# Performance work log

Measured on AMD Instinct MI355X. Metric: run time of the kernel, lower is better.

Reference implementation:

```python
import jax, jax.numpy as jnp
import numpy as np

B = 256      # number of graphs (args.batch_size)
NPG = 1000   # nodes per graph (args.num_node)
C = 64       # in_channels
DEG = 16     # avg degree
K = 500      # ceil(ratio * NPG), ratio = 0.5
EPS = 1e-8


def setup_inputs() -> dict:
    key = jax.random.key(0)
    k1, k2, k3, k4, k5 = jax.random.split(key, 5)
    N = B * NPG
    epg = NPG * DEG  # edges per graph
    x = jax.random.normal(k1, (N, C), jnp.float32)
    src = jax.random.randint(k2, (B, epg), 0, NPG)
    dst = jax.random.randint(k3, (B, epg), 0, NPG)
    off = (jnp.arange(B, dtype=jnp.int32) * NPG)[:, None]
    edge_index = jnp.stack([(src + off).reshape(-1), (dst + off).reshape(-1)]).astype(jnp.int32)
    edge_attr = jax.random.uniform(k4, (B * epg,), jnp.float32)
    batch = jnp.repeat(jnp.arange(B, dtype=jnp.int32), NPG)
    W = jax.random.normal(k5, (C, C), jnp.float32) * (1.0 / np.sqrt(C))
    b = jnp.zeros((C,), jnp.float32)
    return {"istraining": 1, "x": x, "edge_index": edge_index, "edge_attr": edge_attr,
            "batch": batch, "W": W, "b": b}


def _gcn_conv(x, edge_index, W, b):
    # PyG GCNConv: x' = D^{-1/2} (A + I) D^{-1/2} X W + b, unit edge weights.
    N = x.shape[0]
    sl = jnp.arange(N, dtype=edge_index.dtype)
    src = jnp.concatenate([edge_index[0], sl])  # message source j
    dst = jnp.concatenate([edge_index[1], sl])  # aggregation target i
    deg = jnp.zeros((N,), x.dtype).at[dst].add(1.0)
    dinv = jnp.where(deg > 0, jax.lax.rsqrt(jnp.maximum(deg, 1.0)), 0.0)
    norm = dinv[src] * dinv[dst]          # [E+N]
    h = x @ W                              # [N, C]
    msg = h[src] * norm[:, None]           # gather + scale (dominant traffic)
    out = jax.ops.segment_sum(msg, dst, num_segments=N) + b
    return out


def _node_score(x):
    # compute_node_score: cosine similarity of each node to its graph centroid
    # (community prototype), plus KL(softmax(score) || uniform) per graph.
    xb = x.reshape(B, NPG, C)
    cen = xb.mean(axis=1, keepdims=True)                       # [B,1,C]
    num = jnp.sum(xb * cen, axis=-1)                           # [B,NPG]
    den = jnp.linalg.norm(xb, axis=-1) * jnp.linalg.norm(cen, axis=-1) + EPS
    score = num / den                                          # [B,NPG]
    logp = jax.nn.log_softmax(score, axis=1)
    kl = jnp.sum(jnp.exp(logp) * (logp + jnp.log(jnp.float32(NPG))), axis=1)  # [B]
    indices_ = jnp.argsort(-score, axis=1)                     # [B,NPG]
    return score, kl, indices_


def reference(istraining, x, edge_index, edge_attr, batch, W, b):
    N = x.shape[0]
    x = _gcn_conv(x, edge_index, W, b)
    score, kl_all_batch, indices_ = _node_score(x)
    # per-graph top-k (fixed k since every graph has NPG nodes)
    _, idx = jax.lax.top_k(score, K)                           # [B,K]
    perm = ((jnp.arange(B, dtype=idx.dtype) * NPG)[:, None] + idx).reshape(-1)  # [B*K]
    score_flat = score.reshape(-1)
    x_new = x[perm] * jnp.tanh(score_flat[perm])[:, None]
    batch_new = batch[perm]
    # filter_adj: keep edges with both endpoints retained, re-index to new ids.
    mapping = jnp.full((N,), -1, dtype=jnp.int32).at[perm].set(
        jnp.arange(perm.shape[0], dtype=jnp.int32))
    new_ei = mapping[edge_index]                               # [2,E], -1 = dropped
    edge_mask = jnp.logical_and(new_ei[0] >= 0, new_ei[1] >= 0)
    edge_attr_new = jnp.where(edge_mask, edge_attr, 0.0)
    return (x_new, new_ei, edge_attr_new, edge_mask, batch_new, perm, kl_all_batch, indices_)
```

## Files before the change

kernel.cpp:

```cpp
#include <hip/hip_runtime.h>
#include <math.h>

#define NPG 1000
#define KTOP 500
#define C 64
#define EPG 16000
#define BPG 63

__device__ __forceinline__ int readlane_i(int v, int l) {
    return (int)__builtin_amdgcn_readlane((unsigned)v, (unsigned)l);
}

__global__ __launch_bounds__(1024) void build_graph_k(const int* __restrict__ ei, int E,
                                                      int* __restrict__ deg,
                                                      float* __restrict__ dinv,
                                                      int* __restrict__ off,
                                                      int* __restrict__ csr,
                                                      float* __restrict__ cen_sum) {
    int g = blockIdx.x, t = threadIdx.x;
    __shared__ int cnt[NPG];
    __shared__ int soff[NPG];
    __shared__ unsigned short lcsr[EPG];
    __shared__ int red[1024];
    const int gbase = g * NPG;
    const int ebase = g * EPG;
    const int* __restrict__ srcp = ei + ebase;
    const int* __restrict__ dstp = ei + E + ebase;

    if (t < C) cen_sum[(size_t)g * C + t] = 0.f;
    for (int i = t; i < NPG; i += 1024) cnt[i] = 0;
    __syncthreads();
    for (int i = t; i < EPG; i += 1024) atomicAdd(&cnt[dstp[i] - gbase], 1);
    __syncthreads();
    int v = (t < NPG) ? cnt[t] : 0;
    red[t] = v;
    __syncthreads();
    for (int o = 1; o < 1024; o <<= 1) {
        int xx = (t >= o) ? red[t - o] : 0;
        __syncthreads();
        red[t] += xx;
        __syncthreads();
    }
    if (t < NPG) soff[t] = red[t] - v;
    __syncthreads();
    for (int i = t; i < NPG; i += 1024) {
        int d = cnt[i];
        deg[gbase + i] = d;
        dinv[gbase + i] = 1.0f / sqrtf((float)(d + 1));
        off[gbase + i] = ebase + soff[i];
    }
    __syncthreads();
    for (int i = t; i < NPG; i += 1024) cnt[i] = soff[i];
    __syncthreads();
    for (int i = t; i < EPG; i += 1024) {
        int d = dstp[i] - gbase;
        int pos = atomicAdd(&cnt[d], 1);
        lcsr[pos] = (unsigned short)(srcp[i] - gbase);
    }
    __syncthreads();
    int4* co = (int4*)(csr + ebase);
    for (int i = t; i < EPG / 4; i += 1024) {
        int4 vv;
        vv.x = gbase + (int)lcsr[i * 4 + 0];
        vv.y = gbase + (int)lcsr[i * 4 + 1];
        vv.z = gbase + (int)lcsr[i * 4 + 2];
        vv.w = gbase + (int)lcsr[i * 4 + 3];
        co[i] = vv;
    }
}

__global__ __launch_bounds__(256) void gemm_k(const float* __restrict__ x,
                                              const float* __restrict__ W,
                                              const float* __restrict__ dinv,
                                              float* __restrict__ h2, int N) {
    __shared__ float sW[C * C];
    int t = threadIdx.x;
    for (int i = t; i < C * C / 4; i += 256) ((float4*)sW)[i] = ((const float4*)W)[i];
    __syncthreads();
    int r0 = blockIdx.x * 512 + t;
    int r1 = r0 + 256;
    if (r0 >= N) return;
    bool has1 = (r1 < N);
    const float4* x0 = (const float4*)(x + (size_t)r0 * C);
    const float4* x1 = (const float4*)(x + (size_t)(has1 ? r1 : r0) * C);
    float acc0[C], acc1[C];
#pragma unroll
    for (int i = 0; i < C; ++i) { acc0[i] = 0.f; acc1[i] = 0.f; }
    float4 a0 = x0[0], a1 = x1[0];
    for (int k4 = 0; k4 < 16; ++k4) {
        float4 b0, b1;
        if (k4 < 15) { b0 = x0[k4 + 1]; b1 = x1[k4 + 1]; }
        const float4* wr = (const float4*)(sW + k4 * 4 * C);
        const float* a0f = (const float*)&a0;
        const float* a1f = (const float*)&a1;
#pragma unroll
        for (int c4 = 0; c4 < 16; ++c4) {
            float4 w[4];
            w[0] = wr[c4]; w[1] = wr[16 + c4]; w[2] = wr[32 + c4]; w[3] = wr[48 + c4];
            const float* wf = (const float*)w;
#pragma unroll
            for (int j = 0; j < 4; ++j) {
                float s0 = acc0[c4 * 4 + j], s1 = acc1[c4 * 4 + j];
#pragma unroll
                for (int kk = 0; kk < 4; ++kk) {
                    float wv = wf[kk * 4 + j];
                    s0 = fmaf(a0f[kk], wv, s0);
                    s1 = fmaf(a1f[kk], wv, s1);
                }
                acc0[c4 * 4 + j] = s0; acc1[c4 * 4 + j] = s1;
            }
        }
        a0 = b0; a1 = b1;
    }
    float dv0 = dinv[r0];
    float dv1 = has1 ? dinv[r1] : 0.f;
#pragma unroll
    for (int i = 0; i < C; ++i) { acc0[i] *= dv0; acc1[i] *= dv1; }
    float4* h0 = (float4*)(h2 + (size_t)r0 * C);
#pragma unroll
    for (int q = 0; q < 16; ++q) h0[q] = ((float4*)acc0)[q];
    if (has1) {
        float4* h1 = (float4*)(h2 + (size_t)r1 * C);
#pragma unroll
        for (int q = 0; q < 16; ++q) h1[q] = ((float4*)acc1)[q];
    }
}

__global__ __launch_bounds__(256) void gather_k(const int* __restrict__ csr,
                                                const int* __restrict__ off,
                                                const int* __restrict__ deg,
                                                const float* __restrict__ h2,
                                                const float* __restrict__ dinv,
                                                const float* __restrict__ bias,
                                                float* __restrict__ out2,
                                                float* __restrict__ cen_sum,
                                                int N, int B) {
    __shared__ float cenacc[C];
    int blk = blockIdx.x;
    int wave = threadIdx.x >> 6;
    int lane = threadIdx.x & 63;
    int t = threadIdx.x;
    int g, blkin;
    if ((B & 7) == 0) {
        int xcd = blk & 7, slot = blk >> 3;
        g = (slot / BPG) * 8 + xcd;
        blkin = slot % BPG;
    } else {
        g = blk / BPG;
        blkin = blk % BPG;
    }
    if (t < C) cenacc[t] = 0.f;
    __syncthreads();

    int base = blkin * 4 + wave;
    if (base < NPG / 4) {
        int nA = g * NPG + base;
        int nB = nA + 250, nC_ = nA + 500, nD = nA + 750;
        int oA = off[nA], oB = off[nB], oC = off[nC_], oD = off[nD];
        int dA = deg[nA], dB = deg[nB], dC = deg[nC_], dD = deg[nD];
        float diA = dinv[nA], diB = dinv[nB], diC = dinv[nC_], diD = dinv[nD];
        float hA = h2[(size_t)nA * C + lane];
        float hB = h2[(size_t)nB * C + lane];
        float hC = h2[(size_t)nC_ * C + lane];
        float hD = h2[(size_t)nD * C + lane];
        float bv = bias[lane];
        int svA = (lane < dA) ? csr[oA + lane] : nA;
        int svB = (lane < dB) ? csr[oB + lane] : nB;
        int svC = (lane < dC) ? csr[oC + lane] : nC_;
        int svD = (lane < dD) ? csr[oD + lane] : nD;
        int jmA = dA < 64 ? dA : 64;
        int jmB = dB < 64 ? dB : 64;
        int jmC = dC < 64 ? dC : 64;
        int jmD = dD < 64 ? dD : 64;
        int rA = (jmA + 3) & ~3, rB = (jmB + 3) & ~3;
        int rC = (jmC + 3) & ~3, rD = (jmD + 3) & ~3;
        int m0 = rA > rB ? rA : rB;
        int m1 = rC > rD ? rC : rD;
        int mmax = m0 > m1 ? m0 : m1;
        float aA = 0.f, aB = 0.f, aC = 0.f, aD = 0.f;
        for (int j = 0; j < mmax; j += 4) {
            if (j < rA) {
                int s0 = readlane_i(svA, j + 0), s1 = readlane_i(svA, j + 1);
                int s2 = readlane_i(svA, j + 2), s3 = readlane_i(svA, j + 3);
                float v0 = h2[(size_t)s0 * C + lane];
                float v1 = h2[(size_t)s1 * C + lane];
                float v2 = h2[(size_t)s2 * C + lane];
                float v3 = h2[(size_t)s3 * C + lane];
                aA += (v0 + v1) + (v2 + v3);
            }
            if (j < rB) {
                int s0 = readlane_i(svB, j + 0), s1 = readlane_i(svB, j + 1);
                int s2 = readlane_i(svB, j + 2), s3 = readlane_i(svB, j + 3);
                float v0 = h2[(size_t)s0 * C + lane];
                float v1 = h2[(size_t)s1 * C + lane];
                float v2 = h2[(size_t)s2 * C + lane];
                float v3 = h2[(size_t)s3 * C + lane];
                aB += (v0 + v1) + (v2 + v3);
            }
            if (j < rC) {
                int s0 = readlane_i(svC, j + 0), s1 = readlane_i(svC, j + 1);
                int s2 = readlane_i(svC, j + 2), s3 = readlane_i(svC, j + 3);
                float v0 = h2[(size_t)s0 * C + lane];
                float v1 = h2[(size_t)s1 * C + lane];
                float v2 = h2[(size_t)s2 * C + lane];
                float v3 = h2[(size_t)s3 * C + lane];
                aC += (v0 + v1) + (v2 + v3);
            }
            if (j < rD) {
                int s0 = readlane_i(svD, j + 0), s1 = readlane_i(svD, j + 1);
                int s2 = readlane_i(svD, j + 2), s3 = readlane_i(svD, j + 3);
                float v0 = h2[(size_t)s0 * C + lane];
                float v1 = h2[(size_t)s1 * C + lane];
                float v2 = h2[(size_t)s2 * C + lane];
                float v3 = h2[(size_t)s3 * C + lane];
                aD += (v0 + v1) + (v2 + v3);
            }
        }
        for (int j = 64; j < dA; ++j) aA += h2[(size_t)csr[oA + j] * C + lane];
        for (int j = 64; j < dB; ++j) aB += h2[(size_t)csr[oB + j] * C + lane];
        for (int j = 64; j < dC; ++j) aC += h2[(size_t)csr[oC + j] * C + lane];
        for (int j = 64; j < dD; ++j) aD += h2[(size_t)csr[oD + j] * C + lane];
        float cA = 1.0f - (float)(rA - jmA);
        float cB = 1.0f - (float)(rB - jmB);
        float cC = 1.0f - (float)(rC - jmC);
        float cD = 1.0f - (float)(rD - jmD);
        float resA = fmaf(diA, fmaf(cA, hA, aA), bv);
        float resB = fmaf(diB, fmaf(cB, hB, aB), bv);
        float resC = fmaf(diC, fmaf(cC, hC, aC), bv);
        float resD = fmaf(diD, fmaf(cD, hD, aD), bv);
        out2[(size_t)nA * C + lane] = resA;
        out2[(size_t)nB * C + lane] = resB;
        out2[(size_t)nC_ * C + lane] = resC;
        out2[(size_t)nD * C + lane] = resD;
        float csum = (resA + resB) + (resC + resD);
        atomicAdd(&cenacc[lane], csum);
    }
    __syncthreads();
    if (t < C) atomicAdd(&cen_sum[(size_t)g * C + t], cenacc[t]);
}

__global__ void cen_fin_k(const float* __restrict__ cen_sum, float* __restrict__ cen,
                          float* __restrict__ cnorm) {
    int g = blockIdx.x, c = threadIdx.x;
    float m = cen_sum[(size_t)g * C + c] * (1.0f / 1000.0f);
    cen[g * C + c] = m;
    float v = m * m;
    for (int o = 32; o > 0; o >>= 1) v += __shfl_down(v, o, 64);
    if (c == 0) cnorm[g] = sqrtf(v);
}

__global__ __launch_bounds__(256) void score2_k(const float* __restrict__ out2,
                                                const float* __restrict__ cen,
                                                const float* __restrict__ cnorm,
                                                float* __restrict__ score, int N) {
    int wave = threadIdx.x >> 6, lane = threadIdx.x & 63;
    int r0 = blockIdx.x * 16 + wave * 4;
    if (r0 >= N) return;
    int g0 = (r0 + 0) / NPG, g1 = (r0 + 1) / NPG;
    int g2 = (r0 + 2) / NPG, g3 = (r0 + 3) / NPG;
    float m0 = cen[g0 * C + lane];
    float m1 = cen[g1 * C + lane];
    float m2 = cen[g2 * C + lane];
    float m3 = cen[g3 * C + lane];
    float a0 = out2[(size_t)(r0 + 0) * C + lane];
    float a1 = out2[(size_t)(r0 + 1) * C + lane];
    float a2 = out2[(size_t)(r0 + 2) * C + lane];
    float a3 = out2[(size_t)(r0 + 3) * C + lane];
    float n0 = a0 * m0, n1 = a1 * m1, n2 = a2 * m2, n3 = a3 * m3;
    float q0 = a0 * a0, q1 = a1 * a1, q2 = a2 * a2, q3 = a3 * a3;
    for (int o = 32; o > 0; o >>= 1) {
        n0 += __shfl_down(n0, o, 64); q0 += __shfl_down(q0, o, 64);
        n1 += __shfl_down(n1, o, 64); q1 += __shfl_down(q1, o, 64);
        n2 += __shfl_down(n2, o, 64); q2 += __shfl_down(q2, o, 64);
        n3 += __shfl_down(n3, o, 64); q3 += __shfl_down(q3, o, 64);
    }
    if (lane == 0) {
        score[r0 + 0] = n0 / (sqrtf(q0) * cnorm[g0] + 1e-8f);
        score[r0 + 1] = n1 / (sqrtf(q1) * cnorm[g1] + 1e-8f);
        score[r0 + 2] = n2 / (sqrtf(q2) * cnorm[g2] + 1e-8f);
        score[r0 + 3] = n3 / (sqrtf(q3) * cnorm[g3] + 1e-8f);
    }
}

__global__ void softmax_kl_k(const float* __restrict__ score, float* __restrict__ o_kl) {
    int g = blockIdx.x, t = threadIdx.x;
    __shared__ float ss[NPG];
    __shared__ float red[256];
    const float4* s4 = (const float4*)(score + (size_t)g * NPG);
    for (int i = t; i < NPG / 4; i += 256) ((float4*)ss)[i] = s4[i];
    __syncthreads();
    float mx = -INFINITY;
    for (int i = t; i < NPG; i += 256) mx = fmaxf(mx, ss[i]);
    red[t] = mx;
    __syncthreads();
    for (int w = 128; w > 0; w >>= 1) { if (t < w) red[t] = fmaxf(red[t], red[t + w]); __syncthreads(); }
    mx = red[0];
    __syncthreads();
    float se = 0.f;
    for (int i = t; i < NPG; i += 256) se += expf(ss[i] - mx);
    red[t] = se;
    __syncthreads();
    for (int w = 128; w > 0; w >>= 1) { if (t < w) red[t] += red[t + w]; __syncthreads(); }
    float lse = logf(red[0]);
    __syncthreads();
    float kl = 0.f;
    const float ln_npg = 6.9077552790f;
    for (int i = t; i < NPG; i += 256) {
        float lp = ss[i] - mx - lse;
        kl += expf(lp) * (lp + ln_npg);
    }
    red[t] = kl;
    __syncthreads();
    for (int w = 128; w > 0; w >>= 1) { if (t < w) red[t] += red[t + w]; __syncthreads(); }
    if (t == 0) o_kl[g] = red[0];
}

__global__ __launch_bounds__(1024) void sort_k(const float* __restrict__ score,
                                               int* __restrict__ sidx,
                                               int* __restrict__ mapping,
                                               float* __restrict__ o_perm,
                                               float* __restrict__ o_batch,
                                               float* __restrict__ o_ind) {
    __shared__ unsigned long long kk[1024];
    int g = blockIdx.x, t = threadIdx.x;
    const int gbase = g * NPG;
    unsigned long long v;
    if (t < NPG) {
        unsigned u = __float_as_uint(score[(size_t)gbase + t]);
        u = (u & 0x80000000u) ? ~u : (u | 0x80000000u);
        v = ((unsigned long long)(~u) << 32) | (unsigned)t;
    } else {
        v = ~0ULL;
    }
    kk[t] = v;
    __syncthreads();
    for (int k = 2; k <= 1024; k <<= 1) {
        for (int j = k >> 1; j > 0; j >>= 1) {
            int ixj = t ^ j;
            if (ixj > t) {
                unsigned long long a = kk[t], b = kk[ixj];
                bool up = ((t & k) == 0);
                if ((a > b) == up) { kk[t] = b; kk[ixj] = a; }
            }
            __syncthreads();
        }
    }
    if (t < NPG) {
        int node = (int)(kk[t] & 0xFFFFFFFFULL);
        sidx[(size_t)gbase + t] = node;
        o_ind[(size_t)gbase + t] = (float)node;
        mapping[gbase + node] = (t < KTOP) ? (g * KTOP + t) : -1;
        if (t < KTOP) {
            o_perm[(size_t)g * KTOP + t] = (float)(gbase + node);
            o_batch[(size_t)g * KTOP + t] = (float)g;
        }
    }
}

__global__ __launch_bounds__(256) void topk_k(const int* __restrict__ sidx,
                                              const float* __restrict__ score,
                                              const float* __restrict__ out2,
                                              float* __restrict__ o_xnew, int BK) {
    int wave = threadIdx.x >> 6, lane = threadIdx.x & 63;
    int j = blockIdx.x * 4 + wave;
    if (j < BK) {
        int b = j / KTOP, r = j - b * KTOP;
        int node = sidx[(size_t)b * NPG + r];
        int gn = b * NPG + node;
        float tn = tanhf(score[gn]);
        o_xnew[(size_t)j * C + lane] = out2[(size_t)gn * C + lane] * tn;
    }
}

__global__ void edge_out_k(const int* __restrict__ ei, const float* __restrict__ eattr,
                           const int* __restrict__ mapping, float* __restrict__ o_newei,
                           float* __restrict__ o_eattr, float* __restrict__ o_mask, int E) {
    int e4 = blockIdx.x * 256 + threadIdx.x;
    int q = E >> 2;
    if (e4 < q) {
        int4 sidx = ((const int4*)ei)[e4];
        int4 didx = ((const int4*)ei)[q + e4];
        int a0 = mapping[sidx.x], a1 = mapping[sidx.y], a2 = mapping[sidx.z], a3 = mapping[sidx.w];
        int b0 = mapping[didx.x], b1 = mapping[didx.y], b2 = mapping[didx.z], b3 = mapping[didx.w];
        float4 f0 = { (float)a0, (float)a1, (float)a2, (float)a3 };
        float4 f1 = { (float)b0, (float)b1, (float)b2, (float)b3 };
        ((float4*)o_newei)[e4] = f0;
        ((float4*)o_newei)[q + e4] = f1;
        float4 at = ((const float4*)eattr)[e4];
        float4 mk, ea;
        mk.x = (a0 >= 0 && b0 >= 0) ? 1.0f : 0.0f;
        mk.y = (a1 >= 0 && b1 >= 0) ? 1.0f : 0.0f;
        mk.z = (a2 >= 0 && b2 >= 0) ? 1.0f : 0.0f;
        mk.w = (a3 >= 0 && b3 >= 0) ? 1.0f : 0.0f;
        ea.x = mk.x != 0.0f ? at.x : 0.0f;
        ea.y = mk.y != 0.0f ? at.y : 0.0f;
        ea.z = mk.z != 0.0f ? at.z : 0.0f;
        ea.w = mk.w != 0.0f ? at.w : 0.0f;
        ((float4*)o_mask)[e4] = mk;
        ((float4*)o_eattr)[e4] = ea;
    }
}

extern "C" void kernel_launch(void* const* d_in, const int* in_sizes, int n_in,
                              void* d_out, int out_size, void* d_ws, size_t ws_size,
                              hipStream_t stream) {
    (void)n_in; (void)out_size; (void)ws_size;
    const float* x     = (const float*)d_in[1];
    const int*   ei    = (const int*)d_in[2];
    const float* eattr = (const float*)d_in[3];
    const float* W     = (const float*)d_in[5];
    const float* bias  = (const float*)d_in[6];

    const int N  = in_sizes[1] / C;
    const int E  = in_sizes[2] / 2;
    const int B  = N / NPG;
    const int BK = B * KTOP;

    char* wsp = (char*)d_ws;
    float* out2    = (float*)wsp; wsp += (size_t)N * C * 4;
    float* dinv    = (float*)wsp; wsp += (size_t)N * 4;
    int*   deg     = (int*)wsp;   wsp += (size_t)N * 4;
    int*   off     = (int*)wsp;   wsp += (size_t)N * 4;
    int*   mapping = (int*)wsp;   wsp += (size_t)N * 4;
    float* score   = (float*)wsp; wsp += (size_t)N * 4;
    int*   sidx    = (int*)wsp;   wsp += (size_t)N * 4;
    float* cen_sum = (float*)wsp; wsp += (size_t)B * C * 4;
    float* cen     = (float*)wsp; wsp += (size_t)B * C * 4;
    float* cnorm   = (float*)wsp; wsp += 1024;

    float* out     = (float*)d_out;
    float* o_xnew  = out;
    float* o_newei = o_xnew + (size_t)BK * C;
    float* o_eattr = o_newei + 2 * (size_t)E;
    float* o_mask  = o_eattr + (size_t)E;
    float* o_batch = o_mask + (size_t)E;
    float* o_perm  = o_batch + (size_t)BK;
    float* o_kl    = o_perm + (size_t)BK;
    float* o_ind   = o_kl + (size_t)B;

    float* h2buf = out;
    int*   csr   = (int*)o_eattr;

    build_graph_k<<<B, 1024, 0, stream>>>(ei, E, deg, dinv, off, csr, cen_sum);
    gemm_k<<<(N + 511) / 512, 256, 0, stream>>>(x, W, dinv, h2buf, N);
    gather_k<<<B * BPG, 256, 0, stream>>>(csr, off, deg, h2buf, dinv, bias, out2,
                                          cen_sum, N, B);
    cen_fin_k<<<B, 64, 0, stream>>>(cen_sum, cen, cnorm);
    score2_k<<<(N + 15) / 16, 256, 0, stream>>>(out2, cen, cnorm, score, N);
    softmax_kl_k<<<B, 256, 0, stream>>>(score, o_kl);
    sort_k<<<B, 1024, 0, stream>>>(score, sidx, mapping, o_perm, o_batch, o_ind);
    topk_k<<<(BK + 3) / 4, 256, 0, stream>>>(sidx, score, out2, o_xnew, BK);
    edge_out_k<<<(E / 4 + 255) / 256, 256, 0, stream>>>(ei, eattr, mapping,
                                                        o_newei, o_eattr, o_mask, E);
}
```

Before: 414.8 us.

## Use scalar CSR loads in gather, fuse softmax-KL into sort and topk into edge kernel

The gather kernel now makes the row offset and degree wave-uniform with readfirstlane and reads neighbor indices as scalar loads straight from the CSR array. This drops the per-lane index preload, the readlane shuffles and the self-loop padding correction. The softmax/KL reduction moves into the sort kernel so scores are read once, and the top-k gather and edge remapping kernels are merged into one launch, with top-k now handling one node per thread using float4 copies. These changes cut kernel launches and redundant loads, but the top-k path loses its coalesced per-lane stores and the KL reductions add barriers to the sort kernel.

```diff
diff --git a/kernel.cpp b/kernel.cpp
--- a/kernel.cpp
+++ b/kernel.cpp
@@ -7,9 +7,7 @@
 #define EPG 16000
 #define BPG 63
 
-__device__ __forceinline__ int readlane_i(int v, int l) {
-    return (int)__builtin_amdgcn_readlane((unsigned)v, (unsigned)l);
-}
+__device__ __forceinline__ int rfl(int v) { return __builtin_amdgcn_readfirstlane(v); }
 
 __global__ __launch_bounds__(1024) void build_graph_k(const int* __restrict__ ei, int E,
                                                       int* __restrict__ deg,
@@ -156,59 +154,50 @@
     if (base < NPG / 4) {
         int nA = g * NPG + base;
         int nB = nA + 250, nC_ = nA + 500, nD = nA + 750;
-        int oA = off[nA], oB = off[nB], oC = off[nC_], oD = off[nD];
-        int dA = deg[nA], dB = deg[nB], dC = deg[nC_], dD = deg[nD];
+        int oA = rfl(off[nA]), oB = rfl(off[nB]), oC = rfl(off[nC_]), oD = rfl(off[nD]);
+        int dA = rfl(deg[nA]), dB = rfl(deg[nB]), dC = rfl(deg[nC_]), dD = rfl(deg[nD]);
+        const int* __restrict__ cpA = csr + oA;
+        const int* __restrict__ cpB = csr + oB;
+        const int* __restrict__ cpC = csr + oC;
+        const int* __restrict__ cpD = csr + oD;
         float diA = dinv[nA], diB = dinv[nB], diC = dinv[nC_], diD = dinv[nD];
         float hA = h2[(size_t)nA * C + lane];
         float hB = h2[(size_t)nB * C + lane];
         float hC = h2[(size_t)nC_ * C + lane];
         float hD = h2[(size_t)nD * C + lane];
         float bv = bias[lane];
-        int svA = (lane < dA) ? csr[oA + lane] : nA;
-        int svB = (lane < dB) ? csr[oB + lane] : nB;
-        int svC = (lane < dC) ? csr[oC + lane] : nC_;
-        int svD = (lane < dD) ? csr[oD + lane] : nD;
-        int jmA = dA < 64 ? dA : 64;
-        int jmB = dB < 64 ? dB : 64;
-        int jmC = dC < 64 ? dC : 64;
-        int jmD = dD < 64 ? dD : 64;
-        int rA = (jmA + 3) & ~3, rB = (jmB + 3) & ~3;
-        int rC = (jmC + 3) & ~3, rD = (jmD + 3) & ~3;
-        int m0 = rA > rB ? rA : rB;
-        int m1 = rC > rD ? rC : rD;
+        int mA = dA & ~3, mB = dB & ~3, mC = dC & ~3, mD = dD & ~3;
+        int m0 = mA > mB ? mA : mB;
+        int m1 = mC > mD ? mC : mD;
         int mmax = m0 > m1 ? m0 : m1;
         float aA = 0.f, aB = 0.f, aC = 0.f, aD = 0.f;
         for (int j = 0; j < mmax; j += 4) {
-            if (j < rA) {
-                int s0 = readlane_i(svA, j + 0), s1 = readlane_i(svA, j + 1);
-                int s2 = readlane_i(svA, j + 2), s3 = readlane_i(svA, j + 3);
+            if (j < mA) {
+                int s0 = cpA[j + 0], s1 = cpA[j + 1], s2 = cpA[j + 2], s3 = cpA[j + 3];
                 float v0 = h2[(size_t)s0 * C + lane];
                 float v1 = h2[(size_t)s1 * C + lane];
                 float v2 = h2[(size_t)s2 * C + lane];
                 float v3 = h2[(size_t)s3 * C + lane];
                 aA += (v0 + v1) + (v2 + v3);
             }
-            if (j < rB) {
-                int s0 = readlane_i(svB, j + 0), s1 = readlane_i(svB, j + 1);
-                int s2 = readlane_i(svB, j + 2), s3 = readlane_i(svB, j + 3);
+            if (j < mB) {
+                int s0 = cpB[j + 0], s1 = cpB[j + 1], s2 = cpB[j + 2], s3 = cpB[j + 3];
                 float v0 = h2[(size_t)s0 * C + lane];
                 float v1 = h2[(size_t)s1 * C + lane];
                 float v2 = h2[(size_t)s2 * C + lane];
                 float v3 = h2[(size_t)s3 * C + lane];
                 aB += (v0 + v1) + (v2 + v3);
             }
-            if (j < rC) {
-                int s0 = readlane_i(svC, j + 0), s1 = readlane_i(svC, j + 1);
-                int s2 = readlane_i(svC, j + 2), s3 = readlane_i(svC, j + 3);
+            if (j < mC) {
+                int s0 = cpC[j + 0], s1 = cpC[j + 1], s2 = cpC[j + 2], s3 = cpC[j + 3];
                 float v0 = h2[(size_t)s0 * C + lane];
                 float v1 = h2[(size_t)s1 * C + lane];
                 float v2 = h2[(size_t)s2 * C + lane];
                 float v3 = h2[(size_t)s3 * C + lane];
                 aC += (v0 + v1) + (v2 + v3);
             }
-            if (j < rD) {
-                int s0 = readlane_i(svD, j + 0), s1 = readlane_i(svD, j + 1);
-                int s2 = readlane_i(svD, j + 2), s3 = readlane_i(svD, j + 3);
+            if (j < mD) {
+                int s0 = cpD[j + 0], s1 = cpD[j + 1], s2 = cpD[j + 2], s3 = cpD[j + 3];
                 float v0 = h2[(size_t)s0 * C + lane];
                 float v1 = h2[(size_t)s1 * C + lane];
                 float v2 = h2[(size_t)s2 * C + lane];
@@ -216,18 +205,14 @@
                 aD += (v0 + v1) + (v2 + v3);
             }
         }
-        for (int j = 64; j < dA; ++j) aA += h2[(size_t)csr[oA + j] * C + lane];
-        for (int j = 64; j < dB; ++j) aB += h2[(size_t)csr[oB + j] * C + lane];
-        for (int j = 64; j < dC; ++j) aC += h2[(size_t)csr[oC + j] * C + lane];
-        for (int j = 64; j < dD; ++j) aD += h2[(size_t)csr[oD + j] * C + lane];
-        float cA = 1.0f - (float)(rA - jmA);
-        float cB = 1.0f - (float)(rB - jmB);
-        float cC = 1.0f - (float)(rC - jmC);
-        float cD = 1.0f - (float)(rD - jmD);
-        float resA = fmaf(diA, fmaf(cA, hA, aA), bv);
-        float resB = fmaf(diB, fmaf(cB, hB, aB), bv);
-        float resC = fmaf(diC, fmaf(cC, hC, aC), bv);
-        float resD = fmaf(diD, fmaf(cD, hD, aD), bv);
+        for (int j = mA; j < dA; ++j) aA += h2[(size_t)cpA[j] * C + lane];
+        for (int j = mB; j < dB; ++j) aB += h2[(size_t)cpB[j] * C + lane];
+        for (int j = mC; j < dC; ++j) aC += h2[(size_t)cpC[j] * C + lane];
+        for (int j = mD; j < dD; ++j) aD += h2[(size_t)cpD[j] * C + lane];
+        float resA = fmaf(diA, aA + hA, bv);
+        float resB = fmaf(diB, aB + hB, bv);
+        float resC = fmaf(diC, aC + hC, bv);
+        float resD = fmaf(diD, aD + hD, bv);
         out2[(size_t)nA * C + lane] = resA;
         out2[(size_t)nB * C + lane] = resB;
         out2[(size_t)nC_ * C + lane] = resC;
@@ -282,51 +267,42 @@
     }
 }
 
-__global__ void softmax_kl_k(const float* __restrict__ score, float* __restrict__ o_kl) {
-    int g = blockIdx.x, t = threadIdx.x;
-    __shared__ float ss[NPG];
-    __shared__ float red[256];
-    const float4* s4 = (const float4*)(score + (size_t)g * NPG);
-    for (int i = t; i < NPG / 4; i += 256) ((float4*)ss)[i] = s4[i];
-    __syncthreads();
-    float mx = -INFINITY;
-    for (int i = t; i < NPG; i += 256) mx = fmaxf(mx, ss[i]);
-    red[t] = mx;
-    __syncthreads();
-    for (int w = 128; w > 0; w >>= 1) { if (t < w) red[t] = fmaxf(red[t], red[t + w]); __syncthreads(); }
-    mx = red[0];
-    __syncthreads();
-    float se = 0.f;
-    for (int i = t; i < NPG; i += 256) se += expf(ss[i] - mx);
-    red[t] = se;
-    __syncthreads();
-    for (int w = 128; w > 0; w >>= 1) { if (t < w) red[t] += red[t + w]; __syncthreads(); }
-    float lse = logf(red[0]);
-    __syncthreads();
-    float kl = 0.f;
-    const float ln_npg = 6.9077552790f;
-    for (int i = t; i < NPG; i += 256) {
-        float lp = ss[i] - mx - lse;
-        kl += expf(lp) * (lp + ln_npg);
-    }
-    red[t] = kl;
-    __syncthreads();
-    for (int w = 128; w > 0; w >>= 1) { if (t < w) red[t] += red[t + w]; __syncthreads(); }
-    if (t == 0) o_kl[g] = red[0];
-}
-
-__global__ __launch_bounds__(1024) void sort_k(const float* __restrict__ score,
-                                               int* __restrict__ sidx,
-                                               int* __restrict__ mapping,
-                                               float* __restrict__ o_perm,
-                                               float* __restrict__ o_batch,
-                                               float* __restrict__ o_ind) {
+__global__ __launch_bounds__(1024) void sort_kl_k(const float* __restrict__ score,
+                                                  int* __restrict__ sidx,
+                                                  int* __restrict__ mapping,
+                                                  float* __restrict__ o_perm,
+                                                  float* __restrict__ o_batch,
+                                                  float* __restrict__ o_kl,
+                                                  float* __restrict__ o_ind) {
+    __shared__ float red[1024];
     __shared__ unsigned long long kk[1024];
     int g = blockIdx.x, t = threadIdx.x;
     const int gbase = g * NPG;
+    float sv = (t < NPG) ? score[(size_t)gbase + t] : -INFINITY;
+    red[t] = sv;
+    __syncthreads();
+    for (int w = 512; w > 0; w >>= 1) { if (t < w) red[t] = fmaxf(red[t], red[t + w]); __syncthreads(); }
+    float mx = red[0];
+    __syncthreads();
+    float ex = (t < NPG) ? expf(sv - mx) : 0.f;
+    red[t] = ex;
+    __syncthreads();
+    for (int w = 512; w > 0; w >>= 1) { if (t < w) red[t] += red[t + w]; __syncthreads(); }
+    float lse = logf(red[0]);
+    __syncthreads();
+    const float ln_npg = 6.9077552790f;
+    float kl = 0.f;
+    if (t < NPG) {
+        float lp = sv - mx - lse;
+        kl = expf(lp) * (lp + ln_npg);
+    }
+    red[t] = kl;
+    __syncthreads();
+    for (int w = 512; w > 0; w >>= 1) { if (t < w) red[t] += red[t + w]; __syncthreads(); }
+    if (t == 0) o_kl[g] = red[0];
     unsigned long long v;
     if (t < NPG) {
-        unsigned u = __float_as_uint(score[(size_t)gbase + t]);
+        unsigned u = __float_as_uint(sv);
         u = (u & 0x80000000u) ? ~u : (u | 0x80000000u);
         v = ((unsigned long long)(~u) << 32) | (unsigned)t;
     } else {
@@ -357,47 +333,58 @@
     }
 }
 
-__global__ __launch_bounds__(256) void topk_k(const int* __restrict__ sidx,
-                                              const float* __restrict__ score,
-                                              const float* __restrict__ out2,
-                                              float* __restrict__ o_xnew, int BK) {
-    int wave = threadIdx.x >> 6, lane = threadIdx.x & 63;
-    int j = blockIdx.x * 4 + wave;
-    if (j < BK) {
-        int b = j / KTOP, r = j - b * KTOP;
-        int node = sidx[(size_t)b * NPG + r];
-        int gn = b * NPG + node;
-        float tn = tanhf(score[gn]);
-        o_xnew[(size_t)j * C + lane] = out2[(size_t)gn * C + lane] * tn;
-    }
-}
-
-__global__ void edge_out_k(const int* __restrict__ ei, const float* __restrict__ eattr,
-                           const int* __restrict__ mapping, float* __restrict__ o_newei,
-                           float* __restrict__ o_eattr, float* __restrict__ o_mask, int E) {
-    int e4 = blockIdx.x * 256 + threadIdx.x;
-    int q = E >> 2;
-    if (e4 < q) {
-        int4 sidx = ((const int4*)ei)[e4];
-        int4 didx = ((const int4*)ei)[q + e4];
-        int a0 = mapping[sidx.x], a1 = mapping[sidx.y], a2 = mapping[sidx.z], a3 = mapping[sidx.w];
-        int b0 = mapping[didx.x], b1 = mapping[didx.y], b2 = mapping[didx.z], b3 = mapping[didx.w];
-        float4 f0 = { (float)a0, (float)a1, (float)a2, (float)a3 };
-        float4 f1 = { (float)b0, (float)b1, (float)b2, (float)b3 };
-        ((float4*)o_newei)[e4] = f0;
-        ((float4*)o_newei)[q + e4] = f1;
-        float4 at = ((const float4*)eattr)[e4];
-        float4 mk, ea;
-        mk.x = (a0 >= 0 && b0 >= 0) ? 1.0f : 0.0f;
-        mk.y = (a1 >= 0 && b1 >= 0) ? 1.0f : 0.0f;
-        mk.z = (a2 >= 0 && b2 >= 0) ? 1.0f : 0.0f;
-        mk.w = (a3 >= 0 && b3 >= 0) ? 1.0f : 0.0f;
-        ea.x = mk.x != 0.0f ? at.x : 0.0f;
-        ea.y = mk.y != 0.0f ? at.y : 0.0f;
-        ea.z = mk.z != 0.0f ? at.z : 0.0f;
-        ea.w = mk.w != 0.0f ? at.w : 0.0f;
-        ((float4*)o_mask)[e4] = mk;
-        ((float4*)o_eattr)[e4] = ea;
+__global__ __launch_bounds__(256) void topk_edge_k(const int* __restrict__ sidx,
+                                                   const float* __restrict__ score,
+                                                   const float* __restrict__ out2,
+                                                   const int* __restrict__ ei,
+                                                   const float* __restrict__ eattr,
+                                                   const int* __restrict__ mapping,
+                                                   float* __restrict__ o_xnew,
+                                                   float* __restrict__ o_newei,
+                                                   float* __restrict__ o_eattr,
+                                                   float* __restrict__ o_mask,
+                                                   int E, int BK, int TKB) {
+    if (blockIdx.x < (unsigned)TKB) {
+        int j = blockIdx.x * 256 + threadIdx.x;
+        if (j < BK) {
+            int b = j / KTOP, r = j - b * KTOP;
+            int node = sidx[(size_t)b * NPG + r];
+            int gn = b * NPG + node;
+            float tn = tanhf(score[gn]);
+            const float4* src = (const float4*)(out2 + (size_t)gn * C);
+            float4* dst = (float4*)(o_xnew + (size_t)j * C);
+#pragma unroll
+            for (int q = 0; q < 16; ++q) {
+                float4 v = src[q];
+                v.x *= tn; v.y *= tn; v.z *= tn; v.w *= tn;
+                dst[q] = v;
+            }
+        }
+    } else {
+        int e4 = (blockIdx.x - TKB) * 256 + threadIdx.x;
+        int q = E >> 2;
+        if (e4 < q) {
+            int4 sdx = ((const int4*)ei)[e4];
+            int4 ddx = ((const int4*)ei)[q + e4];
+            int a0 = mapping[sdx.x], a1 = mapping[sdx.y], a2 = mapping[sdx.z], a3 = mapping[sdx.w];
+            int b0 = mapping[ddx.x], b1 = mapping[ddx.y], b2 = mapping[ddx.z], b3 = mapping[ddx.w];
+            float4 f0 = { (float)a0, (float)a1, (float)a2, (float)a3 };
+            float4 f1 = { (float)b0, (float)b1, (float)b2, (float)b3 };
+            ((float4*)o_newei)[e4] = f0;
+            ((float4*)o_newei)[q + e4] = f1;
+            float4 at = ((const float4*)eattr)[e4];
+            float4 mk, ea;
+            mk.x = (a0 >= 0 && b0 >= 0) ? 1.0f : 0.0f;
+            mk.y = (a1 >= 0 && b1 >= 0) ? 1.0f : 0.0f;
+            mk.z = (a2 >= 0 && b2 >= 0) ? 1.0f : 0.0f;
+            mk.w = (a3 >= 0 && b3 >= 0) ? 1.0f : 0.0f;
+            ea.x = mk.x != 0.0f ? at.x : 0.0f;
+            ea.y = mk.y != 0.0f ? at.y : 0.0f;
+            ea.z = mk.z != 0.0f ? at.z : 0.0f;
+            ea.w = mk.w != 0.0f ? at.w : 0.0f;
+            ((float4*)o_mask)[e4] = mk;
+            ((float4*)o_eattr)[e4] = ea;
+        }
     }
 }
 
@@ -441,15 +428,17 @@
     float* h2buf = out;
     int*   csr   = (int*)o_eattr;
 
+    const int TKB = (BK + 255) / 256;
+    const int EB  = (E / 4 + 255) / 256;
+
     build_graph_k<<<B, 1024, 0, stream>>>(ei, E, deg, dinv, off, csr, cen_sum);
     gemm_k<<<(N + 511) / 512, 256, 0, stream>>>(x, W, dinv, h2buf, N);
     gather_k<<<B * BPG, 256, 0, stream>>>(csr, off, deg, h2buf, dinv, bias, out2,
                                           cen_sum, N, B);
     cen_fin_k<<<B, 64, 0, stream>>>(cen_sum, cen, cnorm);
     score2_k<<<(N + 15) / 16, 256, 0, stream>>>(out2, cen, cnorm, score, N);
-    softmax_kl_k<<<B, 256, 0, stream>>>(score, o_kl);
-    sort_k<<<B, 1024, 0, stream>>>(score, sidx, mapping, o_perm, o_batch, o_ind);
-    topk_k<<<(BK + 3) / 4, 256, 0, stream>>>(sidx, score, out2, o_xnew, BK);
-    edge_out_k<<<(E / 4 + 255) / 256, 256, 0, stream>>>(ei, eattr, mapping,
-                                                        o_newei, o_eattr, o_mask, E);
-}
+    sort_kl_k<<<B, 1024, 0, stream>>>(score, sidx, mapping, o_perm, o_batch, o_kl, o_ind);
+    topk_edge_k<<<TKB + EB, 256, 0, stream>>>(sidx, score, out2, ei, eattr, mapping,
+                                              o_xnew, o_newei, o_eattr, o_mask,
+                                              E, BK, TKB);
+}
```

Measured after the change: 412.1 us. About the same (-0.6%).
